# Kernel optimization log

Hardware: AMD Instinct MI355X
Metric: run time of the kernel (lower is better)

## Reference

```python
import jax, jax.numpy as jnp
import numpy as np
from jax import lax

N_FFT = 512
HOP = 128
Q = N_FFT // HOP  # 4
KW = 2 * N_FFT - 1  # conv kernel width 1023


def _hann_periodic(n: int) -> np.ndarray:
    # scipy.signal.get_window('hann', n) default fftbins=True -> periodic hann
    k = np.arange(n)
    return (0.5 - 0.5 * np.cos(2.0 * np.pi * k / n)).astype(np.float64)


def _compute_alpha(W: np.ndarray, S: np.ndarray) -> np.ndarray:
    # Faithful port of ConsistencyLoss._compute_alpha (paper eq. 9)
    N, R = N_FFT, HOP
    alpha = np.zeros((2 * Q - 1, 2 * N - 1), dtype=np.complex64)
    for qi, q in enumerate(range(-(Q - 1), Q)):
        S_sh = np.zeros(N)
        s0, s1 = max(0, -q * R), min(N, N - q * R)
        if s0 < s1:
            S_sh[s0:s1] = S[q * R + s0: q * R + s1]
        term = W * S_sh
        f = np.fft.fft(term, 2 * N - 1)
        alpha[qi] = np.fft.fftshift(f) / N
    alpha[Q - 1, N - 1] -= 1.0
    return alpha


def setup_inputs() -> dict:
    key = jax.random.key(0)
    waveform = 0.1 * jax.random.normal(key, (4, 131072), dtype=jnp.float32)
    W_np = _hann_periodic(N_FFT)
    alpha = _compute_alpha(W_np, W_np)
    return {
        "waveform": waveform,
        "window": jnp.asarray(W_np, dtype=jnp.float32),
        "alpha_real": jnp.asarray(alpha.real, dtype=jnp.float32),
        "alpha_imag": jnp.asarray(alpha.imag, dtype=jnp.float32),
    }


def _stft(waveform, window):
    # torch.stft(center=True, pad_mode='reflect', onesided=True), output (B, T, F)
    N, hop = N_FFT, HOP
    B, L = waveform.shape
    padded = jnp.pad(waveform, ((0, 0), (N // 2, N // 2)), mode="reflect")
    T = 1 + L // hop
    idx = hop * jnp.arange(T)[:, None] + jnp.arange(N)[None, :]  # (T, N)
    frames = padded[:, idx] * window  # (B, T, N)
    return jnp.fft.rfft(frames, axis=-1)  # (B, T, N//2+1) complex64


def reference(waveform, window, alpha_real, alpha_imag):
    N, hop = N_FFT, HOP
    B = waveform.shape[0]
    H = _stft(waveform, window)  # (B, T, N//2+1)
    T = H.shape[1]

    # reconstruct full two-sided spectrum: concat conj-flipped interior bins
    H_full = jnp.concatenate([H, jnp.conj(H[:, :, 1:-1][:, :, ::-1])], axis=2)  # (B, T, N)
    H_full = jnp.transpose(H_full, (0, 2, 1))  # (B, N, T)

    # fuse the phase-term einsum into the per-frequency conv kernel:
    # C[b,n,t] = sum_q phase[n,q] * (alpha[q] * H_full[b,n])(t)
    #          = (K_eff[n] * H_full[b,n])(t),  K_eff = phase @ alpha
    q_idx = jnp.arange(-(Q - 1), Q, dtype=jnp.float32)
    n_idx = jnp.arange(N, dtype=jnp.float32)
    phase = jnp.exp(1j * (2.0 * jnp.pi / N) * n_idx[:, None] * q_idx[None, :])  # (N, 2Q-1)
    alpha = alpha_real + 1j * alpha_imag  # (2Q-1, KW)
    K = phase @ alpha.astype(jnp.complex64)  # (N, KW)
    Kr, Ki = jnp.real(K), jnp.imag(K)

    # complex depthwise (groups=N) cross-correlation via real 2-channel trick
    Hri = jnp.stack([jnp.real(H_full), jnp.imag(H_full)], axis=2).reshape(B, 2 * N, T)
    kern = jnp.stack([
        jnp.stack([Kr, -Ki], axis=1),  # real output rows (N, 2, KW)
        jnp.stack([Ki, Kr], axis=1),   # imag output rows (N, 2, KW)
    ], axis=1).reshape(2 * N, 2, KW)
    out = lax.conv_general_dilated(
        Hri, kern, window_strides=(1,), padding=[(N - 1, N - 1)],
        dimension_numbers=("NCH", "OIH", "NCH"), feature_group_count=N,
    )  # (B, 2N, T)
    Cr, Ci = out[:, 0::2], out[:, 1::2]  # (B, N, T)

    loss = jnp.sum(Cr * Cr + Ci * Ci)
    return loss / (B * T)
```

## Files before the change

kernel.cpp:

```cpp
#include <hip/hip_runtime.h>
#include <math.h>

#define T_FRAMES 1025
#define TSTRIDE  1032
#define BATCH    4
#define LWAV     131072
#define KWC      1023
#define MFFT     2048
#define PI_F     3.14159265358979323846f

struct c32 { float r, i; };
__device__ __forceinline__ c32 mkc(float r, float i){ c32 z; z.r=r; z.i=i; return z; }
__device__ __forceinline__ c32 cadd(c32 a, c32 b){ return mkc(a.r+b.r, a.i+b.i); }
__device__ __forceinline__ c32 csub(c32 a, c32 b){ return mkc(a.r-b.r, a.i-b.i); }
__device__ __forceinline__ c32 cmul(c32 a, c32 b){ return mkc(a.r*b.r - a.i*b.i, a.r*b.i + a.i*b.r); }
__device__ __forceinline__ c32 cni(c32 a){ return mkc(a.i, -a.r); }
#define C8F 0.70710678118654752440f
__device__ __forceinline__ c32 c8p(c32 a){ return mkc(C8F*(a.r+a.i), C8F*(a.i-a.r)); }
__device__ __forceinline__ c32 c8m(c32 a){ return mkc(C8F*(a.i-a.r), -C8F*(a.r+a.i)); }

__device__ __forceinline__ void st2(float2* X, int p, c32 v){ X[p] = make_float2(v.r, v.i); }
__device__ __forceinline__ c32 ld2(const float2* X, int p){ float2 e = X[p]; return mkc(e.x, e.y); }

__device__ __forceinline__ int pX(int j){ return j + (j >> 5); }
__device__ __forceinline__ int pS2(int j){ return j + (j >> 4); }
__device__ __forceinline__ int rev9(int j){ return (int)(__brev((unsigned)j) >> 23); }

__device__ __forceinline__ c32 wexp(int r) {
    float s, c;
    __sincosf((float)r * (-PI_F / 1024.0f), &s, &c);
    return mkc(c, s);
}

__device__ __forceinline__ void dif8_tw(c32 y[8], c32 w3) {
    c32 w2 = cmul(w3, w3), w1 = cmul(w2, w2);
    c32 u[8], v[8], d;
    d = csub(y[0], y[4]); u[0] = cadd(y[0], y[4]); u[4] = cmul(d, w3);
    d = csub(y[1], y[5]); u[1] = cadd(y[1], y[5]); u[5] = c8p(cmul(d, w3));
    d = csub(y[2], y[6]); u[2] = cadd(y[2], y[6]); u[6] = cni(cmul(d, w3));
    d = csub(y[3], y[7]); u[3] = cadd(y[3], y[7]); u[7] = c8m(cmul(d, w3));
    d = csub(u[0], u[2]); v[0] = cadd(u[0], u[2]); v[2] = cmul(d, w2);
    d = csub(u[1], u[3]); v[1] = cadd(u[1], u[3]); v[3] = cni(cmul(d, w2));
    d = csub(u[4], u[6]); v[4] = cadd(u[4], u[6]); v[6] = cmul(d, w2);
    d = csub(u[5], u[7]); v[5] = cadd(u[5], u[7]); v[7] = cni(cmul(d, w2));
    d = csub(v[0], v[1]); y[0] = cadd(v[0], v[1]); y[1] = cmul(d, w1);
    d = csub(v[2], v[3]); y[2] = cadd(v[2], v[3]); y[3] = cmul(d, w1);
    d = csub(v[4], v[5]); y[4] = cadd(v[4], v[5]); y[5] = cmul(d, w1);
    d = csub(v[6], v[7]); y[6] = cadd(v[6], v[7]); y[7] = cmul(d, w1);
}
__device__ __forceinline__ void dif8_nt(c32 y[8]) {
    c32 u[8], v[8], d;
    d = csub(y[0], y[4]); u[0] = cadd(y[0], y[4]); u[4] = d;
    d = csub(y[1], y[5]); u[1] = cadd(y[1], y[5]); u[5] = c8p(d);
    d = csub(y[2], y[6]); u[2] = cadd(y[2], y[6]); u[6] = cni(d);
    d = csub(y[3], y[7]); u[3] = cadd(y[3], y[7]); u[7] = c8m(d);
    d = csub(u[0], u[2]); v[0] = cadd(u[0], u[2]); v[2] = d;
    d = csub(u[1], u[3]); v[1] = cadd(u[1], u[3]); v[3] = cni(d);
    d = csub(u[4], u[6]); v[4] = cadd(u[4], u[6]); v[6] = d;
    d = csub(u[5], u[7]); v[5] = cadd(u[5], u[7]); v[7] = cni(d);
    d = csub(v[0], v[1]); y[0] = cadd(v[0], v[1]); y[1] = d;
    d = csub(v[2], v[3]); y[2] = cadd(v[2], v[3]); y[3] = d;
    d = csub(v[4], v[5]); y[4] = cadd(v[4], v[5]); y[5] = d;
    d = csub(v[6], v[7]); y[6] = cadd(v[6], v[7]); y[7] = d;
}
__device__ __forceinline__ void dit8_tw(c32 y[8], c32 w3) {
    c32 w2 = cmul(w3, w3), w1 = cmul(w2, w2);
    c32 u[8], v[8], t;
    t = cmul(y[1], w1); u[0] = cadd(y[0], t); u[1] = csub(y[0], t);
    t = cmul(y[3], w1); u[2] = cadd(y[2], t); u[3] = csub(y[2], t);
    t = cmul(y[5], w1); u[4] = cadd(y[4], t); u[5] = csub(y[4], t);
    t = cmul(y[7], w1); u[6] = cadd(y[6], t); u[7] = csub(y[6], t);
    t = cmul(u[2], w2);      v[0] = cadd(u[0], t); v[2] = csub(u[0], t);
    t = cni(cmul(u[3], w2)); v[1] = cadd(u[1], t); v[3] = csub(u[1], t);
    t = cmul(u[6], w2);      v[4] = cadd(u[4], t); v[6] = csub(u[4], t);
    t = cni(cmul(u[7], w2)); v[5] = cadd(u[5], t); v[7] = csub(u[5], t);
    t = cmul(v[4], w3);      y[0] = cadd(v[0], t); y[4] = csub(v[0], t);
    t = c8p(cmul(v[5], w3)); y[1] = cadd(v[1], t); y[5] = csub(v[1], t);
    t = cni(cmul(v[6], w3)); y[2] = cadd(v[2], t); y[6] = csub(v[2], t);
    t = c8m(cmul(v[7], w3)); y[3] = cadd(v[3], t); y[7] = csub(v[3], t);
}
__device__ __forceinline__ void dit8_nt(c32 y[8]) {
    c32 u[8], v[8], t;
    u[0] = cadd(y[0], y[1]); u[1] = csub(y[0], y[1]);
    u[2] = cadd(y[2], y[3]); u[3] = csub(y[2], y[3]);
    u[4] = cadd(y[4], y[5]); u[5] = csub(y[4], y[5]);
    u[6] = cadd(y[6], y[7]); u[7] = csub(y[6], y[7]);
    t = u[2];      v[0] = cadd(u[0], t); v[2] = csub(u[0], t);
    t = cni(u[3]); v[1] = cadd(u[1], t); v[3] = csub(u[1], t);
    t = u[6];      v[4] = cadd(u[4], t); v[6] = csub(u[4], t);
    t = cni(u[7]); v[5] = cadd(u[5], t); v[7] = csub(u[5], t);
    t = v[4];      y[0] = cadd(v[0], t); y[4] = csub(v[0], t);
    t = c8p(v[5]); y[1] = cadd(v[1], t); y[5] = csub(v[1], t);
    t = cni(v[6]); y[2] = cadd(v[2], t); y[6] = csub(v[2], t);
    t = c8m(v[7]); y[3] = cadd(v[3], t); y[7] = csub(v[3], t);
}
__device__ __forceinline__ void dif4(c32 y[4]) {
    c32 u0 = cadd(y[0], y[2]), d0 = csub(y[0], y[2]);
    c32 u1 = cadd(y[1], y[3]), d1 = cni(csub(y[1], y[3]));
    y[0] = cadd(u0, u1); y[1] = csub(u0, u1);
    y[2] = cadd(d0, d1); y[3] = csub(d0, d1);
}
__device__ __forceinline__ void dif4_tw(c32 y[4], c32 w) {
    c32 w2 = cmul(w, w), w3 = cmul(w2, w);
    c32 s0 = cadd(y[0], y[2]), d0 = csub(y[0], y[2]);
    c32 s1 = cadd(y[1], y[3]), d1 = cni(csub(y[1], y[3]));
    y[0] = cadd(s0, s1);
    y[1] = cmul(csub(s0, s1), w2);
    y[2] = cmul(cadd(d0, d1), w);
    y[3] = cmul(csub(d0, d1), w3);
}
__device__ __forceinline__ void dit4(c32 y[4], c32 w) {
    c32 w2 = cmul(w, w);
    c32 t1 = cmul(y[1], w2); c32 u0 = cadd(y[0], t1), u1 = csub(y[0], t1);
    c32 t3 = cmul(y[3], w2); c32 u2 = cadd(y[2], t3), u3 = csub(y[2], t3);
    c32 s2 = cmul(u2, w);      y[0] = cadd(u0, s2); y[2] = csub(u0, s2);
    c32 s3 = cni(cmul(u3, w)); y[1] = cadd(u1, s3); y[3] = csub(u1, s3);
}

#define FSTR 546
__global__ __launch_bounds__(256) void stage1_kernel(const float* __restrict__ wave,
                                                     const float* __restrict__ win,
                                                     const float* __restrict__ ar,
                                                     const float* __restrict__ ai,
                                                     float2* __restrict__ Ht,
                                                     float2* __restrict__ Afbr,
                                                     float* __restrict__ out) {
    __shared__ float2 S2[4368];
    const int tid = threadIdx.x;

    if (blockIdx.x < 516) {
        float2* F = S2;
        const int w = tid >> 6, l = tid & 63;
        const int b = blockIdx.x / 129;
        const int t0 = (blockIdx.x - b * 129) << 3;
        const float* wb = wave + (size_t)b * LWAV;

        for (int pass = 0; pass < 2; ++pass) {
            const int j = w + (pass << 2);
            const int t = t0 + j;
            if (t < T_FRAMES) {
                c32 y[8];
#pragma unroll
                for (int k = 0; k < 8; ++k) {
                    int s = l + (k << 6);
                    int posn = t * 128 + s - 256;
                    int ix = posn < 0 ? -posn : (posn >= LWAV ? 2 * LWAV - 2 - posn : posn);
                    y[k] = mkc(wb[ix] * win[s], 0.f);
                }
                dif8_tw(y, wexp(l << 2));
#pragma unroll
                for (int k = 0; k < 8; ++k) st2(F, j*FSTR + pS2(l + (k << 6)), y[k]);
                __builtin_amdgcn_wave_barrier();
                {
                    int base = ((l >> 3) << 6) + (l & 7);
#pragma unroll
                    for (int k = 0; k < 8; ++k) y[k] = ld2(F, j*FSTR + pS2(base + (k << 3)));
                    dif8_tw(y, wexp((l & 7) << 5));
#pragma unroll
                    for (int k = 0; k < 8; ++k) st2(F, j*FSTR + pS2(base + (k << 3)), y[k]);
                }
                __builtin_amdgcn_wave_barrier();
                {
#pragma unroll
                    for (int k = 0; k < 8; ++k) y[k] = ld2(F, j*FSTR + pS2((l << 3) + k));
                    dif8_nt(y);
#pragma unroll
                    for (int k = 0; k < 8; ++k) st2(F, j*FSTR + pS2((l << 3) + k), y[k]);
                }
            }
        }
        __syncthreads();
        const int jj = tid & 7;
        const int rb = tid >> 3;
        const bool tok = (t0 + jj < T_FRAMES);
        if (tok) {
#pragma unroll
            for (int rr = 0; rr < 8; ++rr) {
                int p = ((rr << 5) + rb) << 1;
                Ht[(size_t)(b * 512 + p) * TSTRIDE + t0 + jj] = F[jj*FSTR + pS2(p)];
            }
            if (tid < 8)
                Ht[(size_t)(b * 512 + 1) * TSTRIDE + t0 + jj] = F[jj*FSTR + pS2(1)];
        }
    } else if (blockIdx.x < 523) {
        float2* X = S2;
        const int q = blockIdx.x - 516;
        c32 y[8];
#pragma unroll
        for (int k = 0; k < 8; ++k) {
            int j = tid + (k << 8);
            y[k] = (j < KWC) ? mkc(ar[q * KWC + j], -ai[q * KWC + j]) : mkc(0.f, 0.f);
        }
        dif8_tw(y, wexp(tid));
#pragma unroll
        for (int k = 0; k < 8; ++k) st2(X, pX(tid + (k << 8)), y[k]);
        __syncthreads();
        {
            int base = ((tid >> 5) << 8) + (tid & 31);
#pragma unroll
            for (int k = 0; k < 8; ++k) y[k] = ld2(X, pX(base + (k << 5)));
            dif8_tw(y, wexp((tid & 31) << 3));
#pragma unroll
            for (int k = 0; k < 8; ++k) st2(X, pX(base + (k << 5)), y[k]);
        }
        __syncthreads();
        {
            int base = ((tid & 63) << 5) + (tid >> 6);
#pragma unroll
            for (int k = 0; k < 8; ++k) y[k] = ld2(X, pX(base + (k << 2)));
            dif8_tw(y, wexp((tid >> 6) << 6));
#pragma unroll
            for (int k = 0; k < 8; ++k) st2(X, pX(base + (k << 2)), y[k]);
        }
        __syncthreads();
#pragma unroll
        for (int h = 0; h < 2; ++h) {
            int g = tid + (h << 8);
            c32 z4[4];
#pragma unroll
            for (int k = 0; k < 4; ++k) z4[k] = ld2(X, pX((g << 2) + k));
            dif4(z4);
#pragma unroll
            for (int k = 0; k < 4; ++k) {
                int jx = (g << 2) + k;
                int j4 = jx >> 1, lo = jx & 1;
                int wv4 = j4 >> 8, rem = j4 & 255;
                int r = rem >> 5, c = (rem >> 2) & 7, kk = rem & 3;
                int s = (wv4 << 8) | (kk << 6) | (r << 3) | c;
                Afbr[(q << 11) + (s << 1) + lo] = make_float2(z4[k].r, -z4[k].i);
            }
        }
    } else {
        if (tid == 0) *out = 0.f;
    }
}

__global__ __launch_bounds__(256) void conv_kernel(const float2* __restrict__ Ht,
                                                   const float2* __restrict__ Afbr,
                                                   float* __restrict__ out) {
    __shared__ float2 S2[4224];
    __shared__ float red[4];
    float2* X0 = S2;
    float2* X1 = S2 + 2112;
    const int tid = threadIdx.x;
    const int l = tid & 63, wv = tid >> 6;
    const int g = blockIdx.x;
    const int half = g / 257;
    const int n = g - half * 257;
    const int b0 = half << 1;
    const int pr = rev9(n);

    const float2* row0 = Ht + (size_t)(b0 * 512 + pr) * TSTRIDE;
    const float2* row1 = Ht + (size_t)((b0 + 1) * 512 + pr) * TSTRIDE;

    const c32 wA  = wexp(tid);
    const c32 wB  = wexp((l & 31) << 3);
    const c32 wP3 = wexp((l & 7) << 5);
    const c32 wI2 = wexp((l & 3) << 6);

    c32 y0[8], y1[8];
#pragma unroll
    for (int k = 0; k < 4; ++k) {
        float2 h0 = row0[tid + (k << 8)]; y0[k] = mkc(h0.x, h0.y);
        float2 h1 = row1[tid + (k << 8)]; y1[k] = mkc(h1.x, h1.y);
    }
    if (tid == 0) {
        float2 h0 = row0[1024]; y0[4] = mkc(h0.x, h0.y);
        float2 h1 = row1[1024]; y1[4] = mkc(h1.x, h1.y);
    } else { y0[4] = mkc(0.f, 0.f); y1[4] = mkc(0.f, 0.f); }
#pragma unroll
    for (int k = 5; k < 8; ++k) { y0[k] = mkc(0.f, 0.f); y1[k] = mkc(0.f, 0.f); }
    dif8_tw(y0, wA);
    dif8_tw(y1, wA);
#pragma unroll
    for (int k = 0; k < 8; ++k) {
        int p = pX(tid + (k << 8));
        st2(X0, p, y0[k]); st2(X1, p, y1[k]);
    }
    __syncthreads();

    const float4* af4 = (const float4*)Afbr;
    const int abase = (wv << 8) + l;
    float4 A[4][7];
#pragma unroll
    for (int kk = 0; kk < 4; ++kk)
#pragma unroll
        for (int qq = 0; qq < 7; ++qq)
            A[kk][qq] = af4[(qq << 10) + abase + (kk << 6)];

    const int Bb = (((wv << 1) + (l >> 5)) << 8) + (l & 31);
#pragma unroll
    for (int gg = 0; gg < 2; ++gg)
#pragma unroll
        for (int t = 0; t < 4; ++t) {
            int p = pX(Bb + (gg << 5) + (t << 6));
            y0[gg*4+t] = ld2(X0, p); y1[gg*4+t] = ld2(X1, p);
        }
    {
        c32 wg1 = c8p(wB);
        dif4_tw(&y0[0], wB); dif4_tw(&y0[4], wg1);
        dif4_tw(&y1[0], wB); dif4_tw(&y1[4], wg1);
    }
#pragma unroll
    for (int gg = 0; gg < 2; ++gg)
#pragma unroll
        for (int t = 0; t < 4; ++t) {
            int p = pX(Bb + (gg << 5) + (t << 6));
            st2(X0, p, y0[gg*4+t]); st2(X1, p, y1[gg*4+t]);
        }
    __builtin_amdgcn_wave_barrier();

    const int chunk = wv << 9;
    const int p3b = chunk + ((l >> 3) << 6) + (l & 7);
#pragma unroll
    for (int u = 0; u < 8; ++u) {
        int p = pX(p3b + (u << 3));
        y0[u] = ld2(X0, p); y1[u] = ld2(X1, p);
    }
    dif8_tw(y0, wP3);
    dif8_tw(y1, wP3);
#pragma unroll
    for (int u = 0; u < 8; ++u) {
        int p = pX(p3b + (u << 3));
        st2(X0, p, y0[u]); st2(X1, p, y1[u]);
    }
    __builtin_amdgcn_wave_barrier();

    const int pos0 = chunk + ((l >> 3) << 6) + ((l & 7) << 3);
    const int px0 = pX(pos0);
#pragma unroll
    for (int u = 0; u < 8; ++u) { y0[u] = ld2(X0, px0 + u); y1[u] = ld2(X1, px0 + u); }
    dif8_nt(y0);
    dif8_nt(y1);
    {
        c32 p1 = wexp(-(n << 2));
        c32 p2 = cmul(p1, p1);
        c32 p3 = cmul(p2, p1);
#pragma unroll
        for (int k = 0; k < 8; ++k) {
            const int kk = k >> 1;
            float4 a;
            c32 Kk;
            a = A[kk][3];
            float ax = (k & 1) ? a.z : a.x, ay = (k & 1) ? a.w : a.y;
            Kk = mkc(ax, ay);
            a = A[kk][4]; ax = (k & 1) ? a.z : a.x; ay = (k & 1) ? a.w : a.y;
            Kk.r += p1.r * ax - p1.i * ay;  Kk.i += p1.r * ay + p1.i * ax;
            a = A[kk][2]; ax = (k & 1) ? a.z : a.x; ay = (k & 1) ? a.w : a.y;
            Kk.r += p1.r * ax + p1.i * ay;  Kk.i += p1.r * ay - p1.i * ax;
            a = A[kk][5]; ax = (k & 1) ? a.z : a.x; ay = (k & 1) ? a.w : a.y;
            Kk.r += p2.r * ax - p2.i * ay;  Kk.i += p2.r * ay + p2.i * ax;
            a = A[kk][1]; ax = (k & 1) ? a.z : a.x; ay = (k & 1) ? a.w : a.y;
            Kk.r += p2.r * ax + p2.i * ay;  Kk.i += p2.r * ay - p2.i * ax;
            a = A[kk][6]; ax = (k & 1) ? a.z : a.x; ay = (k & 1) ? a.w : a.y;
            Kk.r += p3.r * ax - p3.i * ay;  Kk.i += p3.r * ay + p3.i * ax;
            a = A[kk][0]; ax = (k & 1) ? a.z : a.x; ay = (k & 1) ? a.w : a.y;
            Kk.r += p3.r * ax + p3.i * ay;  Kk.i += p3.r * ay - p3.i * ax;
            c32 P0 = cmul(y0[k], Kk);
            c32 P1 = cmul(y1[k], Kk);
            y0[k] = mkc(P0.r, -P0.i);
            y1[k] = mkc(P1.r, -P1.i);
        }
    }
    dit8_nt(y0);
    dit8_nt(y1);
#pragma unroll
    for (int u = 0; u < 8; ++u) { st2(X0, px0 + u, y0[u]); st2(X1, px0 + u, y1[u]); }
    __builtin_amdgcn_wave_barrier();

    const int i2b = chunk + ((l >> 2) << 5) + (l & 3);
#pragma unroll
    for (int gg = 0; gg < 2; ++gg)
#pragma unroll
        for (int t = 0; t < 4; ++t) {
            int p = pX(i2b + (gg << 2) + (t << 3));
            y0[gg*4+t] = ld2(X0, p); y1[gg*4+t] = ld2(X1, p);
        }
    {
        c32 wg1 = c8p(wI2);
        dit4(&y0[0], wI2); dit4(&y0[4], wg1);
        dit4(&y1[0], wI2); dit4(&y1[4], wg1);
    }
#pragma unroll
    for (int gg = 0; gg < 2; ++gg)
#pragma unroll
        for (int t = 0; t < 4; ++t) {
            int p = pX(i2b + (gg << 2) + (t << 3));
            st2(X0, p, y0[gg*4+t]); st2(X1, p, y1[gg*4+t]);
        }
    __builtin_amdgcn_wave_barrier();

    const int i3b = chunk + ((l >> 5) << 8) + (l & 31);
#pragma unroll
    for (int k = 0; k < 8; ++k) {
        int p = pX(i3b + (k << 5));
        y0[k] = ld2(X0, p); y1[k] = ld2(X1, p);
    }
    dit8_tw(y0, wB);
    dit8_tw(y1, wB);
#pragma unroll
    for (int k = 0; k < 8; ++k) {
        int p = pX(i3b + (k << 5));
        st2(X0, p, y0[k]); st2(X1, p, y1[k]);
    }
    __syncthreads();

#pragma unroll
    for (int k = 0; k < 8; ++k) {
        int p = pX(tid + (k << 8));
        y0[k] = ld2(X0, p); y1[k] = ld2(X1, p);
    }
    dit8_tw(y0, wA);
    dit8_tw(y1, wA);
    float local = y0[0].r*y0[0].r + y0[0].i*y0[0].i + y1[0].r*y1[0].r + y1[0].i*y1[0].i
                + y0[1].r*y0[1].r + y0[1].i*y0[1].i + y1[1].r*y1[1].r + y1[1].i*y1[1].i
                + y0[7].r*y0[7].r + y0[7].i*y0[7].i + y1[7].r*y1[7].r + y1[7].i*y1[7].i;
    if (tid < 2)  local += y0[2].r*y0[2].r + y0[2].i*y0[2].i + y1[2].r*y1[2].r + y1[2].i*y1[2].i;
    if (tid >= 1) local += y0[6].r*y0[6].r + y0[6].i*y0[6].i + y1[6].r*y1[6].r + y1[6].i*y1[6].i;

    local *= (n == 0 || n == 256) ? 1.0f : 2.0f;
#pragma unroll
    for (int off = 32; off >= 1; off >>= 1) local += __shfl_down(local, off);
    if ((tid & 63) == 0) red[tid >> 6] = local;
    __syncthreads();
    if (tid == 0) {
        const float SCALE =
            (float)(1.0 / ((double)MFFT * (double)MFFT * (double)BATCH * (double)T_FRAMES));
        atomicAdd(out, (red[0] + red[1] + red[2] + red[3]) * SCALE);
    }
}

extern "C" void kernel_launch(void* const* d_in, const int* in_sizes, int n_in,
                              void* d_out, int out_size, void* d_ws, size_t ws_size,
                              hipStream_t stream) {
    (void)in_sizes; (void)n_in; (void)out_size; (void)ws_size;
    const float* wave   = (const float*)d_in[0];
    const float* window = (const float*)d_in[1];
    const float* ar     = (const float*)d_in[2];
    const float* ai     = (const float*)d_in[3];
    float* out = (float*)d_out;

    char* ws = (char*)d_ws;
    float2* Ht   = (float2*)ws;
    float2* Afbr = (float2*)(ws + 16908288);

    stage1_kernel<<<524, 256, 0, stream>>>(wave, window, ar, ai, Ht, Afbr, out);
    conv_kernel<<<2 * 257, 256, 0, stream>>>(Ht, Afbr, out);
}
```

Before: 85.18 us.

## Process the two batch rows sequentially and stream alpha loads to cut registers

Each FFT stage of the conv kernel now handles the two batch rows one after another in non-unrolled loops instead of interleaving them, and the 28 float4 alpha coefficients are read from global memory inside the multiply stage instead of being preloaded into registers. The aim is to cut VGPR pressure and raise occupancy. In exchange, per-wave instruction-level parallelism drops, the serial per-row loops add overhead, and alpha is now loaded twice per block on the critical path, with no early prefetch to hide the latency.

```diff
diff --git a/kernel.cpp b/kernel.cpp
--- a/kernel.cpp
+++ b/kernel.cpp
@@ -240,8 +240,6 @@
                                                    float* __restrict__ out) {
     __shared__ float2 S2[4224];
     __shared__ float red[4];
-    float2* X0 = S2;
-    float2* X1 = S2 + 2112;
     const int tid = threadIdx.x;
     const int l = tid & 63, wv = tid >> 6;
     const int g = blockIdx.x;
@@ -250,174 +248,147 @@
     const int b0 = half << 1;
     const int pr = rev9(n);
 
-    const float2* row0 = Ht + (size_t)(b0 * 512 + pr) * TSTRIDE;
-    const float2* row1 = Ht + (size_t)((b0 + 1) * 512 + pr) * TSTRIDE;
-
     const c32 wA  = wexp(tid);
     const c32 wB  = wexp((l & 31) << 3);
     const c32 wP3 = wexp((l & 7) << 5);
     const c32 wI2 = wexp((l & 3) << 6);
-
-    c32 y0[8], y1[8];
-#pragma unroll
-    for (int k = 0; k < 4; ++k) {
-        float2 h0 = row0[tid + (k << 8)]; y0[k] = mkc(h0.x, h0.y);
-        float2 h1 = row1[tid + (k << 8)]; y1[k] = mkc(h1.x, h1.y);
-    }
-    if (tid == 0) {
-        float2 h0 = row0[1024]; y0[4] = mkc(h0.x, h0.y);
-        float2 h1 = row1[1024]; y1[4] = mkc(h1.x, h1.y);
-    } else { y0[4] = mkc(0.f, 0.f); y1[4] = mkc(0.f, 0.f); }
-#pragma unroll
-    for (int k = 5; k < 8; ++k) { y0[k] = mkc(0.f, 0.f); y1[k] = mkc(0.f, 0.f); }
-    dif8_tw(y0, wA);
-    dif8_tw(y1, wA);
-#pragma unroll
-    for (int k = 0; k < 8; ++k) {
-        int p = pX(tid + (k << 8));
-        st2(X0, p, y0[k]); st2(X1, p, y1[k]);
+    const c32 wg1B = c8p(wB);
+    const c32 wg1I = c8p(wI2);
+    const c32 p1 = wexp(-(n << 2));
+    const c32 p2 = cmul(p1, p1);
+    const c32 p3 = cmul(p2, p1);
+
+    const int Bb   = (((wv << 1) + (l >> 5)) << 8) + (l & 31);
+    const int chunk = wv << 9;
+    const int p3b  = chunk + ((l >> 3) << 6) + (l & 7);
+    const int pos0 = chunk + ((l >> 3) << 6) + ((l & 7) << 3);
+    const int px0  = pX(pos0);
+    const int i2b  = chunk + ((l >> 2) << 5) + (l & 3);
+    const int i3b  = chunk + ((l >> 5) << 8) + (l & 31);
+    const int abase = (wv << 8) + l;
+    const float4* af4 = (const float4*)Afbr;
+
+#pragma unroll 1
+    for (int r = 0; r < 2; ++r) {
+        const float2* row = Ht + (size_t)((b0 + r) * 512 + pr) * TSTRIDE;
+        float2* X = S2 + r * 2112;
+        c32 y[8];
+#pragma unroll
+        for (int k = 0; k < 4; ++k) { float2 h = row[tid + (k << 8)]; y[k] = mkc(h.x, h.y); }
+        if (tid == 0) { float2 h = row[1024]; y[4] = mkc(h.x, h.y); } else y[4] = mkc(0.f, 0.f);
+        y[5] = mkc(0.f, 0.f); y[6] = mkc(0.f, 0.f); y[7] = mkc(0.f, 0.f);
+        dif8_tw(y, wA);
+#pragma unroll
+        for (int k = 0; k < 8; ++k) st2(X, pX(tid + (k << 8)), y[k]);
     }
     __syncthreads();
 
-    const float4* af4 = (const float4*)Afbr;
-    const int abase = (wv << 8) + l;
-    float4 A[4][7];
-#pragma unroll
-    for (int kk = 0; kk < 4; ++kk)
-#pragma unroll
-        for (int qq = 0; qq < 7; ++qq)
-            A[kk][qq] = af4[(qq << 10) + abase + (kk << 6)];
-
-    const int Bb = (((wv << 1) + (l >> 5)) << 8) + (l & 31);
-#pragma unroll
-    for (int gg = 0; gg < 2; ++gg)
-#pragma unroll
-        for (int t = 0; t < 4; ++t) {
-            int p = pX(Bb + (gg << 5) + (t << 6));
-            y0[gg*4+t] = ld2(X0, p); y1[gg*4+t] = ld2(X1, p);
-        }
-    {
-        c32 wg1 = c8p(wB);
-        dif4_tw(&y0[0], wB); dif4_tw(&y0[4], wg1);
-        dif4_tw(&y1[0], wB); dif4_tw(&y1[4], wg1);
-    }
-#pragma unroll
-    for (int gg = 0; gg < 2; ++gg)
-#pragma unroll
-        for (int t = 0; t < 4; ++t) {
-            int p = pX(Bb + (gg << 5) + (t << 6));
-            st2(X0, p, y0[gg*4+t]); st2(X1, p, y1[gg*4+t]);
-        }
+#pragma unroll 1
+    for (int r = 0; r < 2; ++r) {
+        float2* X = S2 + r * 2112;
+        c32 y[8];
+#pragma unroll
+        for (int gg = 0; gg < 2; ++gg)
+#pragma unroll
+            for (int t = 0; t < 4; ++t) y[gg*4+t] = ld2(X, pX(Bb + (gg << 5) + (t << 6)));
+        dif4_tw(&y[0], wB); dif4_tw(&y[4], wg1B);
+#pragma unroll
+        for (int gg = 0; gg < 2; ++gg)
+#pragma unroll
+            for (int t = 0; t < 4; ++t) st2(X, pX(Bb + (gg << 5) + (t << 6)), y[gg*4+t]);
+    }
     __builtin_amdgcn_wave_barrier();
 
-    const int chunk = wv << 9;
-    const int p3b = chunk + ((l >> 3) << 6) + (l & 7);
-#pragma unroll
-    for (int u = 0; u < 8; ++u) {
-        int p = pX(p3b + (u << 3));
-        y0[u] = ld2(X0, p); y1[u] = ld2(X1, p);
-    }
-    dif8_tw(y0, wP3);
-    dif8_tw(y1, wP3);
-#pragma unroll
-    for (int u = 0; u < 8; ++u) {
-        int p = pX(p3b + (u << 3));
-        st2(X0, p, y0[u]); st2(X1, p, y1[u]);
+#pragma unroll 1
+    for (int r = 0; r < 2; ++r) {
+        float2* X = S2 + r * 2112;
+        c32 y[8];
+#pragma unroll
+        for (int u = 0; u < 8; ++u) y[u] = ld2(X, pX(p3b + (u << 3)));
+        dif8_tw(y, wP3);
+#pragma unroll
+        for (int u = 0; u < 8; ++u) st2(X, pX(p3b + (u << 3)), y[u]);
     }
     __builtin_amdgcn_wave_barrier();
 
-    const int pos0 = chunk + ((l >> 3) << 6) + ((l & 7) << 3);
-    const int px0 = pX(pos0);
-#pragma unroll
-    for (int u = 0; u < 8; ++u) { y0[u] = ld2(X0, px0 + u); y1[u] = ld2(X1, px0 + u); }
-    dif8_nt(y0);
-    dif8_nt(y1);
-    {
-        c32 p1 = wexp(-(n << 2));
-        c32 p2 = cmul(p1, p1);
-        c32 p3 = cmul(p2, p1);
+#pragma unroll 1
+    for (int r = 0; r < 2; ++r) {
+        float2* X = S2 + r * 2112;
+        c32 y[8];
+#pragma unroll
+        for (int u = 0; u < 8; ++u) y[u] = ld2(X, px0 + u);
+        dif8_nt(y);
 #pragma unroll
         for (int k = 0; k < 8; ++k) {
             const int kk = k >> 1;
             float4 a;
             c32 Kk;
-            a = A[kk][3];
+            a = af4[(3 << 10) + abase + (kk << 6)];
             float ax = (k & 1) ? a.z : a.x, ay = (k & 1) ? a.w : a.y;
             Kk = mkc(ax, ay);
-            a = A[kk][4]; ax = (k & 1) ? a.z : a.x; ay = (k & 1) ? a.w : a.y;
+            a = af4[(4 << 10) + abase + (kk << 6)]; ax = (k & 1) ? a.z : a.x; ay = (k & 1) ? a.w : a.y;
             Kk.r += p1.r * ax - p1.i * ay;  Kk.i += p1.r * ay + p1.i * ax;
-            a = A[kk][2]; ax = (k & 1) ? a.z : a.x; ay = (k & 1) ? a.w : a.y;
+            a = af4[(2 << 10) + abase + (kk << 6)]; ax = (k & 1) ? a.z : a.x; ay = (k & 1) ? a.w : a.y;
             Kk.r += p1.r * ax + p1.i * ay;  Kk.i += p1.r * ay - p1.i * ax;
-            a = A[kk][5]; ax = (k & 1) ? a.z : a.x; ay = (k & 1) ? a.w : a.y;
+            a = af4[(5 << 10) + abase + (kk << 6)]; ax = (k & 1) ? a.z : a.x; ay = (k & 1) ? a.w : a.y;
             Kk.r += p2.r * ax - p2.i * ay;  Kk.i += p2.r * ay + p2.i * ax;
-            a = A[kk][1]; ax = (k & 1) ? a.z : a.x; ay = (k & 1) ? a.w : a.y;
+            a = af4[(1 << 10) + abase + (kk << 6)]; ax = (k & 1) ? a.z : a.x; ay = (k & 1) ? a.w : a.y;
             Kk.r += p2.r * ax + p2.i * ay;  Kk.i += p2.r * ay - p2.i * ax;
-            a = A[kk][6]; ax = (k & 1) ? a.z : a.x; ay = (k & 1) ? a.w : a.y;
+            a = af4[(6 << 10) + abase + (kk << 6)]; ax = (k & 1) ? a.z : a.x; ay = (k & 1) ? a.w : a.y;
             Kk.r += p3.r * ax - p3.i * ay;  Kk.i += p3.r * ay + p3.i * ax;
-            a = A[kk][0]; ax = (k & 1) ? a.z : a.x; ay = (k & 1) ? a.w : a.y;
+            a = af4[(0 << 10) + abase + (kk << 6)]; ax = (k & 1) ? a.z : a.x; ay = (k & 1) ? a.w : a.y;
             Kk.r += p3.r * ax + p3.i * ay;  Kk.i += p3.r * ay - p3.i * ax;
-            c32 P0 = cmul(y0[k], Kk);
-            c32 P1 = cmul(y1[k], Kk);
-            y0[k] = mkc(P0.r, -P0.i);
-            y1[k] = mkc(P1.r, -P1.i);
-        }
-    }
-    dit8_nt(y0);
-    dit8_nt(y1);
-#pragma unroll
-    for (int u = 0; u < 8; ++u) { st2(X0, px0 + u, y0[u]); st2(X1, px0 + u, y1[u]); }
+            c32 P = cmul(y[k], Kk);
+            y[k] = mkc(P.r, -P.i);
+        }
+        dit8_nt(y);
+#pragma unroll
+        for (int u = 0; u < 8; ++u) st2(X, px0 + u, y[u]);
+    }
     __builtin_amdgcn_wave_barrier();
 
-    const int i2b = chunk + ((l >> 2) << 5) + (l & 3);
-#pragma unroll
-    for (int gg = 0; gg < 2; ++gg)
-#pragma unroll
-        for (int t = 0; t < 4; ++t) {
-            int p = pX(i2b + (gg << 2) + (t << 3));
-            y0[gg*4+t] = ld2(X0, p); y1[gg*4+t] = ld2(X1, p);
-        }
-    {
-        c32 wg1 = c8p(wI2);
-        dit4(&y0[0], wI2); dit4(&y0[4], wg1);
-        dit4(&y1[0], wI2); dit4(&y1[4], wg1);
-    }
-#pragma unroll
-    for (int gg = 0; gg < 2; ++gg)
-#pragma unroll
-        for (int t = 0; t < 4; ++t) {
-            int p = pX(i2b + (gg << 2) + (t << 3));
-            st2(X0, p, y0[gg*4+t]); st2(X1, p, y1[gg*4+t]);
-        }
+#pragma unroll 1
+    for (int r = 0; r < 2; ++r) {
+        float2* X = S2 + r * 2112;
+        c32 y[8];
+#pragma unroll
+        for (int gg = 0; gg < 2; ++gg)
+#pragma unroll
+            for (int t = 0; t < 4; ++t) y[gg*4+t] = ld2(X, pX(i2b + (gg << 2) + (t << 3)));
+        dit4(&y[0], wI2); dit4(&y[4], wg1I);
+#pragma unroll
+        for (int gg = 0; gg < 2; ++gg)
+#pragma unroll
+            for (int t = 0; t < 4; ++t) st2(X, pX(i2b + (gg << 2) + (t << 3)), y[gg*4+t]);
+    }
     __builtin_amdgcn_wave_barrier();
 
-    const int i3b = chunk + ((l >> 5) << 8) + (l & 31);
-#pragma unroll
-    for (int k = 0; k < 8; ++k) {
-        int p = pX(i3b + (k << 5));
-        y0[k] = ld2(X0, p); y1[k] = ld2(X1, p);
-    }
-    dit8_tw(y0, wB);
-    dit8_tw(y1, wB);
-#pragma unroll
-    for (int k = 0; k < 8; ++k) {
-        int p = pX(i3b + (k << 5));
-        st2(X0, p, y0[k]); st2(X1, p, y1[k]);
+#pragma unroll 1
+    for (int r = 0; r < 2; ++r) {
+        float2* X = S2 + r * 2112;
+        c32 y[8];
+#pragma unroll
+        for (int k = 0; k < 8; ++k) y[k] = ld2(X, pX(i3b + (k << 5)));
+        dit8_tw(y, wB);
+#pragma unroll
+        for (int k = 0; k < 8; ++k) st2(X, pX(i3b + (k << 5)), y[k]);
     }
     __syncthreads();
 
-#pragma unroll
-    for (int k = 0; k < 8; ++k) {
-        int p = pX(tid + (k << 8));
-        y0[k] = ld2(X0, p); y1[k] = ld2(X1, p);
-    }
-    dit8_tw(y0, wA);
-    dit8_tw(y1, wA);
-    float local = y0[0].r*y0[0].r + y0[0].i*y0[0].i + y1[0].r*y1[0].r + y1[0].i*y1[0].i
-                + y0[1].r*y0[1].r + y0[1].i*y0[1].i + y1[1].r*y1[1].r + y1[1].i*y1[1].i
-                + y0[7].r*y0[7].r + y0[7].i*y0[7].i + y1[7].r*y1[7].r + y1[7].i*y1[7].i;
-    if (tid < 2)  local += y0[2].r*y0[2].r + y0[2].i*y0[2].i + y1[2].r*y1[2].r + y1[2].i*y1[2].i;
-    if (tid >= 1) local += y0[6].r*y0[6].r + y0[6].i*y0[6].i + y1[6].r*y1[6].r + y1[6].i*y1[6].i;
-
+    float local = 0.f;
+#pragma unroll 1
+    for (int r = 0; r < 2; ++r) {
+        float2* X = S2 + r * 2112;
+        c32 y[8];
+#pragma unroll
+        for (int k = 0; k < 8; ++k) y[k] = ld2(X, pX(tid + (k << 8)));
+        dit8_tw(y, wA);
+        local += y[0].r*y[0].r + y[0].i*y[0].i
+               + y[1].r*y[1].r + y[1].i*y[1].i
+               + y[7].r*y[7].r + y[7].i*y[7].i;
+        if (tid < 2)  local += y[2].r*y[2].r + y[2].i*y[2].i;
+        if (tid >= 1) local += y[6].r*y[6].r + y[6].i*y[6].i;
+    }
     local *= (n == 0 || n == 256) ? 1.0f : 2.0f;
 #pragma unroll
     for (int off = 32; off >= 1; off >>= 1) local += __shfl_down(local, off);
```

New measurement: 84.75 us. Within noise of the previous version (-0.5%).
